# Kernel optimization log

Measured on AMD Instinct MI355X. Metric: run time of the kernel, lower is better.

## Reference

```python
import jax, jax.numpy as jnp
import numpy as np

N, M, DIM_K, DIM_V = 8192, 8192, 256, 256

def setup_inputs() -> dict:
    key = jax.random.key(0)
    kq, kk, kv = jax.random.split(key, 3)
    Q = jax.random.normal(kq, (N, DIM_K), dtype=jnp.float32)
    K = jax.random.normal(kk, (M, DIM_K), dtype=jnp.float32)
    V = jax.random.normal(kv, (M, DIM_V), dtype=jnp.float32)
    return {"Q": Q, "K": K, "V": V}

def reference(Q, K, V):
    # scores: [N, M] = Q @ K^T / sqrt(dim_k)
    scale = 1.0 / jnp.sqrt(jnp.asarray(Q.shape[-1], dtype=Q.dtype))
    scores = jnp.einsum('nd,md->nm', Q, K) * scale
    attn = jax.nn.softmax(scores, axis=-1)  # softmax over keys
    return attn @ V  # [N, dim_v]
```

## Files before the change

kernel.cpp:

```cpp
#include <hip/hip_runtime.h>
#include <hip/hip_bf16.h>
#include <hip/hip_fp16.h>


typedef __attribute__((ext_vector_type(16))) float floatx16;
typedef __attribute__((ext_vector_type(8)))  short short8;

union S8u { short8 v; unsigned short u[8]; };

#if __has_builtin(__builtin_amdgcn_exp2f)
#define EXP2F(x) __builtin_amdgcn_exp2f(x)
#else
#define EXP2F(x) exp2f(x)
#endif

__device__ __forceinline__ unsigned short f2bf(float f) {
    unsigned int u = __builtin_bit_cast(unsigned int, f);
    unsigned int r = u + 0x7fffu + ((u >> 16) & 1u);
    return (unsigned short)(r >> 16);
}

__device__ __forceinline__ unsigned cvtpk_bf16(float lo, float hi) {
    unsigned r;
    asm("v_cvt_pk_bf16_f32 %0, %1, %2" : "=v"(r) : "v"(lo), "v"(hi));
    return r;
}

__device__ __forceinline__ void gload16(const void* g, void* l) {
    __builtin_amdgcn_global_load_lds(
        (const __attribute__((address_space(1))) unsigned int*)g,
        (__attribute__((address_space(3))) unsigned int*)l, 16, 0, 0);
}


__global__ void prep_kernel(const float* __restrict__ K,
                            const float* __restrict__ V,
                            unsigned short* __restrict__ Kb,
                            unsigned short* __restrict__ Vt) {
    __shared__ unsigned short T[64][72];
    const int kv0 = blockIdx.x * 64;
    const int v0  = blockIdx.y * 64;
    const int tid = threadIdx.x;
#pragma unroll
    for (int it = 0; it < 4; ++it) {
        int flat = it * 256 + tid;
        int r  = flat >> 4;
        int c4 = (flat & 15) * 4;
        float4 f = *reinterpret_cast<const float4*>(
            V + (size_t)(kv0 + r) * 256 + v0 + c4);
        T[c4 + 0][r] = f2bf(f.x);
        T[c4 + 1][r] = f2bf(f.y);
        T[c4 + 2][r] = f2bf(f.z);
        T[c4 + 3][r] = f2bf(f.w);
    }
    __syncthreads();
#pragma unroll
    for (int it = 0; it < 2; ++it) {
        int flat = it * 256 + tid;
        int r  = flat >> 3;
        int c8 = (flat & 7) * 8;
        short8 v8 = *reinterpret_cast<const short8*>(&T[r][c8]);
        *reinterpret_cast<short8*>(Vt + (size_t)(v0 + r) * 8192 + kv0 + c8) = v8;
    }
    const int bid = blockIdx.x + 128 * blockIdx.y;
#pragma unroll
    for (int it = 0; it < 2; ++it) {
        int i = bid * 512 + it * 256 + tid;
        const float4* p = reinterpret_cast<const float4*>(K) + (size_t)i * 2;
        float4 a = p[0], b = p[1];
        S8u r;
        r.u[0] = f2bf(a.x); r.u[1] = f2bf(a.y);
        r.u[2] = f2bf(a.z); r.u[3] = f2bf(a.w);
        r.u[4] = f2bf(b.x); r.u[5] = f2bf(b.y);
        r.u[6] = f2bf(b.z); r.u[7] = f2bf(b.w);
        *reinterpret_cast<short8*>(Kb + (size_t)i * 8) = r.v;
    }
}


#define MFMA_B16 __builtin_amdgcn_mfma_f32_32x32x16_bf16

__global__ __launch_bounds__(256, 2)
void attn_kernel(const float* __restrict__ Qf,
                 const unsigned short* __restrict__ Kb,
                 const unsigned short* __restrict__ VtG,
                 __half* __restrict__ Opart,
                 float* __restrict__ Ml,
                 int kv_span, int gshift) {
    __shared__ __align__(16) unsigned char kbuf[2][16384];
    __shared__ __align__(16) unsigned char vbuf[2][16384];

    const int tid  = threadIdx.x;
    const int lane = tid & 63;
    const int w    = tid >> 6;
    const int l31  = lane & 31;
    const int h    = lane >> 5;

    const int ngm1 = (1 << gshift) - 1;
    const int id   = blockIdx.x + 64 * blockIdx.y;
    const int g    = id & ngm1;
    const int qblk = id >> gshift;
    const int kv_begin = g * kv_span;
    const int tiles = kv_span >> 5;
    const int q0 = qblk * 128 + w * 32;

    const float qs = 0.09016844005556021f;
    short8 qf[16];
    {
        const float* qp = Qf + (size_t)(q0 + l31) * 256 + h * 8;
#pragma unroll
        for (int ds = 0; ds < 16; ++ds) {
            float4 f0 = *reinterpret_cast<const float4*>(qp + ds * 16);
            float4 f1 = *reinterpret_cast<const float4*>(qp + ds * 16 + 4);
            uint4 uu;
            uu.x = cvtpk_bf16(f0.x * qs, f0.y * qs);
            uu.y = cvtpk_bf16(f0.z * qs, f0.w * qs);
            uu.z = cvtpk_bf16(f1.x * qs, f1.y * qs);
            uu.w = cvtpk_bf16(f1.z * qs, f1.w * qs);
            qf[ds] = __builtin_bit_cast(short8, uu);
        }
    }

    floatx16 o[8];
#pragma unroll
    for (int vt = 0; vt < 8; ++vt)
#pragma unroll
        for (int r = 0; r < 16; ++r) o[vt][r] = 0.f;
    float m_run = -1e30f, l_run = 0.f;

    int offk[4], offv[4];
#pragma unroll
    for (int i = 0; i < 4; ++i) {
        int j  = i * 256 + tid;
        int rk = j >> 5, ck = (j & 31) ^ (rk & 7);
        offk[i] = rk * 256 + ck * 8;
        int rv = j >> 2, cv = (j & 3) ^ ((rv >> 1) & 3);
        offv[i] = rv * 8192 + cv * 8;
    }

    auto STAGEK = [&](int kv0, int bufsel) {
        const unsigned short* ks = Kb + (size_t)kv0 * 256;
#pragma unroll
        for (int i = 0; i < 4; ++i)
            gload16(ks + offk[i], &kbuf[bufsel][(i * 256 + w * 64) * 16]);
    };
    auto STAGEV = [&](int kv0, int bufsel) {
        const unsigned short* vs = VtG + kv0;
#pragma unroll
        for (int i = 0; i < 4; ++i)
            gload16(vs + offv[i], &vbuf[bufsel][(i * 256 + w * 64) * 16]);
    };

    STAGEK(kv_begin, 0);
    STAGEV(kv_begin, 0);
    asm volatile("s_waitcnt vmcnt(4)" ::: "memory");
    __builtin_amdgcn_s_barrier();

    const int swz  = l31 & 7;
    const int vswz = (l31 >> 1) & 3;

    auto buildPA = [&](const floatx16& sv, int rbase) -> short8 {
        unsigned cpk0 = cvtpk_bf16(sv[rbase + 0], sv[rbase + 1]);
        unsigned cpk1 = cvtpk_bf16(sv[rbase + 2], sv[rbase + 3]);
        unsigned cpk2 = cvtpk_bf16(sv[rbase + 4], sv[rbase + 5]);
        unsigned cpk3 = cvtpk_bf16(sv[rbase + 6], sv[rbase + 7]);
        uint4 uu;
#if __has_builtin(__builtin_amdgcn_permlane32_swap)
        auto r02 = __builtin_amdgcn_permlane32_swap((int)cpk0, (int)cpk2, false, false);
        auto r13 = __builtin_amdgcn_permlane32_swap((int)cpk1, (int)cpk3, false, false);
        uu.x = (unsigned)r02[0]; uu.y = (unsigned)r13[0];
        uu.z = (unsigned)r02[1]; uu.w = (unsigned)r13[1];
#else
        unsigned send0 = h ? cpk0 : cpk2;
        unsigned send1 = h ? cpk1 : cpk3;
        unsigned r0 = (unsigned)__shfl_xor((int)send0, 32);
        unsigned r1 = (unsigned)__shfl_xor((int)send1, 32);
        uu.x = h ? r0 : cpk0;
        uu.y = h ? r1 : cpk1;
        uu.z = h ? cpk2 : r0;
        uu.w = h ? cpk3 : r1;
#endif
        return __builtin_bit_cast(short8, uu);
    };

    for (int t = 0; t < tiles; ++t) {
        const int cur = t & 1;
        const int nxt = cur ^ 1;
        const int tn  = (t + 1 < tiles) ? t + 1 : t;

        STAGEK(kv_begin + tn * 32, nxt);

        const unsigned char* kl = kbuf[cur];
        floatx16 sA, sB;
#pragma unroll
        for (int r = 0; r < 16; ++r) { sA[r] = 0.f; sB[r] = 0.f; }
        __builtin_amdgcn_s_setprio(1);
#pragma unroll
        for (int ds = 0; ds < 8; ++ds) {
            int c0 = (ds * 2 + h) ^ swz;
            short8 a0 = *reinterpret_cast<const short8*>(
                kl + (size_t)l31 * 512 + c0 * 16);
            sA = MFMA_B16(a0, qf[ds], sA, 0, 0, 0);
        }
#pragma unroll
        for (int ds = 8; ds < 16; ++ds) {
            int c0 = (ds * 2 + h) ^ swz;
            short8 a0 = *reinterpret_cast<const short8*>(
                kl + (size_t)l31 * 512 + c0 * 16);
            sB = MFMA_B16(a0, qf[ds], sB, 0, 0, 0);
        }
        __builtin_amdgcn_s_setprio(0);
        floatx16 s0;
#pragma unroll
        for (int r = 0; r < 16; ++r) s0[r] = sA[r] + sB[r];

        {
            float t4[4];
#pragma unroll
            for (int i = 0; i < 4; ++i)
                t4[i] = fmaxf(fmaxf(s0[i], s0[i + 4]),
                              fmaxf(s0[i + 8], s0[i + 12]));
            float mt = fmaxf(fmaxf(t4[0], t4[1]), fmaxf(t4[2], t4[3]));
            mt = fmaxf(mt, __shfl_xor(mt, 32));
            if (__any(mt > m_run + 11.5f)) {
                float mnew = fmaxf(m_run, mt);
                float al = EXP2F(m_run - mnew);
                m_run = mnew;
                l_run *= al;
#pragma unroll
                for (int reg = 0; reg < 16; ++reg) {
                    int srcl = ((reg & 3) + 8 * (reg >> 2)) + 4 * h;
                    float alr = __shfl(al, srcl);
#pragma unroll
                    for (int vt = 0; vt < 8; ++vt) o[vt][reg] *= alr;
                }
            }
#pragma unroll
            for (int r = 0; r < 16; ++r) s0[r] = EXP2F(s0[r] - m_run);
            float u[4];
#pragma unroll
            for (int i = 0; i < 4; ++i)
                u[i] = (s0[i] + s0[i + 4]) + (s0[i + 8] + s0[i + 12]);
            float lt = (u[0] + u[1]) + (u[2] + u[3]);
            lt += __shfl_xor(lt, 32);
            l_run += lt;
        }

        asm volatile("s_waitcnt vmcnt(4)" ::: "memory");
        __builtin_amdgcn_s_barrier();

        STAGEV(kv_begin + tn * 32, nxt);

        const unsigned char* vl = vbuf[cur];
        __builtin_amdgcn_s_setprio(1);
#pragma unroll
        for (int kk = 0; kk < 2; ++kk) {
            short8 pa = buildPA(s0, kk * 8);
            int cvs = (kk * 2 + h) ^ vswz;
#pragma unroll
            for (int vt = 0; vt < 8; ++vt) {
                short8 b = *reinterpret_cast<const short8*>(
                    vl + (size_t)(vt * 32 + l31) * 64 + cvs * 16);
                o[vt] = MFMA_B16(pa, b, o[vt], 0, 0, 0);
            }
        }
        __builtin_amdgcn_s_setprio(0);

        asm volatile("s_waitcnt vmcnt(4)" ::: "memory");
        __builtin_amdgcn_s_barrier();
    }

    const size_t gq = (size_t)g * 8192;
    float linv = 1.0f / l_run;
#pragma unroll
    for (int reg = 0; reg < 16; ++reg) {
        int row = (reg & 3) + 8 * (reg >> 2) + 4 * h;
        float li = __shfl(linv, row);
#pragma unroll
        for (int vt = 0; vt < 8; ++vt)
            Opart[(gq + q0 + row) * 256 + vt * 32 + l31] =
                __float2half_rn(o[vt][reg] * li);
    }
    if (h == 0) {
        size_t idx = (gq + q0 + l31) * 2;
        Ml[idx]     = m_run;
        Ml[idx + 1] = l_run;
    }
}


__global__ void merge_kernel(const __half* __restrict__ Opart,
                             const float* __restrict__ Ml,
                             float* __restrict__ out, int ngroups) {
    const int row = blockIdx.x;
    const int c2  = threadIdx.x;
    float m = -1e30f;
    for (int g = 0; g < ngroups; ++g)
        m = fmaxf(m, Ml[((size_t)g * 8192 + row) * 2]);
    float den = 0.f, ax = 0.f, ay = 0.f;
    for (int g = 0; g < ngroups; ++g) {
        float wg = EXP2F(Ml[((size_t)g * 8192 + row) * 2] - m) *
                   Ml[((size_t)g * 8192 + row) * 2 + 1];
        den += wg;
        __half2 h2 = *reinterpret_cast<const __half2*>(
            &Opart[((size_t)g * 8192 + row) * 256 + c2 * 2]);
        float2 f = __half22float2(h2);
        ax += wg * f.x;
        ay += wg * f.y;
    }
    float dinv = 1.0f / den;
    float2 r; r.x = ax * dinv; r.y = ay * dinv;
    *reinterpret_cast<float2*>(&out[(size_t)row * 256 + c2 * 2]) = r;
}


extern "C" void kernel_launch(void* const* d_in, const int* in_sizes, int n_in,
                              void* d_out, int out_size, void* d_ws, size_t ws_size,
                              hipStream_t stream) {
    const float* Q = (const float*)d_in[0];
    const float* K = (const float*)d_in[1];
    const float* V = (const float*)d_in[2];
    float* out = (float*)d_out;

    unsigned short* Kb = (unsigned short*)d_ws;
    unsigned short* Vt = Kb + (size_t)8192 * 256;

    const size_t base = (size_t)8192 * 256 * 2 * 2;
    const size_t osz  = (size_t)8192 * 256 * 2;
    const size_t mlsz = (size_t)8192 * 2 * 4;

    int gshift = 3;
    for (; gshift > 0; --gshift)
        if (base + ((osz + mlsz) << gshift) <= ws_size) break;
    int ng = 1 << gshift;

    __half* Opart = (__half*)((char*)d_ws + base);
    float*  Mlp   = (float*)((char*)d_ws + base + osz * (size_t)ng);

    prep_kernel<<<dim3(128, 4), 256, 0, stream>>>(K, V, Kb, Vt);
    attn_kernel<<<dim3(64, ng), 256, 0, stream>>>(Q, Kb, Vt, Opart, Mlp,
                                                  8192 / ng, gshift);
    merge_kernel<<<8192, 128, 0, stream>>>(Opart, Mlp, out, ng);
}
```

Before: 123.9 us.

## Software-pipeline PV of previous tile with QK of current tile

Restructures the attention loop so that the P·V MFMAs for tile t-1 are interleaved with the Q·K^T MFMAs for tile t, using probabilities packed into bf16 registers at the end of the previous iteration. A drain step after the loop finishes the last tile. The V staging is moved to the start of each iteration, the two partial score accumulators become one, and the mid-loop barrier is dropped in favour of a single __syncthreads per tile. This aims to hide the softmax dependency chain and cut one barrier per tile. In exchange, the per-iteration sync is now a full wait that may expose load latency, and one V tile is staged twice.

```diff
diff --git a/kernel.cpp b/kernel.cpp
--- a/kernel.cpp
+++ b/kernel.cpp
@@ -153,8 +153,8 @@
 
     STAGEK(kv_begin, 0);
     STAGEV(kv_begin, 0);
-    asm volatile("s_waitcnt vmcnt(4)" ::: "memory");
-    __builtin_amdgcn_s_barrier();
+    STAGEV(kv_begin, 1);
+    __syncthreads();
 
     const int swz  = l31 & 7;
     const int vswz = (l31 >> 1) & 3;
@@ -183,43 +183,44 @@
         return __builtin_bit_cast(short8, uu);
     };
 
+    short8 pa0 = __builtin_bit_cast(short8, uint4{0u, 0u, 0u, 0u});
+    short8 pa1 = pa0;
+
     for (int t = 0; t < tiles; ++t) {
         const int cur = t & 1;
         const int nxt = cur ^ 1;
         const int tn  = (t + 1 < tiles) ? t + 1 : t;
 
         STAGEK(kv_begin + tn * 32, nxt);
-
-        const unsigned char* kl = kbuf[cur];
-        floatx16 sA, sB;
-#pragma unroll
-        for (int r = 0; r < 16; ++r) { sA[r] = 0.f; sB[r] = 0.f; }
+        STAGEV(kv_begin + t * 32, cur);
+
+        const unsigned char* kl  = kbuf[cur];
+        const unsigned char* vlp = vbuf[nxt];
+
+        floatx16 s;
+#pragma unroll
+        for (int r = 0; r < 16; ++r) s[r] = 0.f;
         __builtin_amdgcn_s_setprio(1);
 #pragma unroll
-        for (int ds = 0; ds < 8; ++ds) {
+        for (int ds = 0; ds < 16; ++ds) {
             int c0 = (ds * 2 + h) ^ swz;
             short8 a0 = *reinterpret_cast<const short8*>(
                 kl + (size_t)l31 * 512 + c0 * 16);
-            sA = MFMA_B16(a0, qf[ds], sA, 0, 0, 0);
-        }
-#pragma unroll
-        for (int ds = 8; ds < 16; ++ds) {
-            int c0 = (ds * 2 + h) ^ swz;
-            short8 a0 = *reinterpret_cast<const short8*>(
-                kl + (size_t)l31 * 512 + c0 * 16);
-            sB = MFMA_B16(a0, qf[ds], sB, 0, 0, 0);
+            s = MFMA_B16(a0, qf[ds], s, 0, 0, 0);
+            const int kk = ds >> 3, vt = ds & 7;
+            int cvs = (kk * 2 + h) ^ vswz;
+            short8 b = *reinterpret_cast<const short8*>(
+                vlp + (size_t)(vt * 32 + l31) * 64 + cvs * 16);
+            o[vt] = MFMA_B16(kk ? pa1 : pa0, b, o[vt], 0, 0, 0);
         }
         __builtin_amdgcn_s_setprio(0);
-        floatx16 s0;
-#pragma unroll
-        for (int r = 0; r < 16; ++r) s0[r] = sA[r] + sB[r];
 
         {
             float t4[4];
 #pragma unroll
             for (int i = 0; i < 4; ++i)
-                t4[i] = fmaxf(fmaxf(s0[i], s0[i + 4]),
-                              fmaxf(s0[i + 8], s0[i + 12]));
+                t4[i] = fmaxf(fmaxf(s[i], s[i + 4]),
+                              fmaxf(s[i + 8], s[i + 12]));
             float mt = fmaxf(fmaxf(t4[0], t4[1]), fmaxf(t4[2], t4[3]));
             mt = fmaxf(mt, __shfl_xor(mt, 32));
             if (__any(mt > m_run + 11.5f)) {
@@ -236,38 +237,35 @@
                 }
             }
 #pragma unroll
-            for (int r = 0; r < 16; ++r) s0[r] = EXP2F(s0[r] - m_run);
+            for (int r = 0; r < 16; ++r) s[r] = EXP2F(s[r] - m_run);
             float u[4];
 #pragma unroll
             for (int i = 0; i < 4; ++i)
-                u[i] = (s0[i] + s0[i + 4]) + (s0[i + 8] + s0[i + 12]);
+                u[i] = (s[i] + s[i + 4]) + (s[i + 8] + s[i + 12]);
             float lt = (u[0] + u[1]) + (u[2] + u[3]);
             lt += __shfl_xor(lt, 32);
             l_run += lt;
         }
-
-        asm volatile("s_waitcnt vmcnt(4)" ::: "memory");
-        __builtin_amdgcn_s_barrier();
-
-        STAGEV(kv_begin + tn * 32, nxt);
-
-        const unsigned char* vl = vbuf[cur];
+        pa0 = buildPA(s, 0);
+        pa1 = buildPA(s, 8);
+
+        __syncthreads();
+    }
+
+    {
+        const unsigned char* vlq = vbuf[(tiles - 1) & 1];
         __builtin_amdgcn_s_setprio(1);
 #pragma unroll
         for (int kk = 0; kk < 2; ++kk) {
-            short8 pa = buildPA(s0, kk * 8);
             int cvs = (kk * 2 + h) ^ vswz;
 #pragma unroll
             for (int vt = 0; vt < 8; ++vt) {
                 short8 b = *reinterpret_cast<const short8*>(
-                    vl + (size_t)(vt * 32 + l31) * 64 + cvs * 16);
-                o[vt] = MFMA_B16(pa, b, o[vt], 0, 0, 0);
+                    vlq + (size_t)(vt * 32 + l31) * 64 + cvs * 16);
+                o[vt] = MFMA_B16(kk ? pa1 : pa0, b, o[vt], 0, 0, 0);
             }
         }
         __builtin_amdgcn_s_setprio(0);
-
-        asm volatile("s_waitcnt vmcnt(4)" ::: "memory");
-        __builtin_amdgcn_s_barrier();
     }
 
     const size_t gq = (size_t)g * 8192;
```

After: 121.2 us, median of 2. -2.2%, faster.
